# Optimization experiments

Measured on AMD Instinct MI355X. Metric: run time of the kernel, lower is better.

The kernel has to match this reference:

```python
import jax, jax.numpy as jnp
import numpy as np

B, N, C_X, D_MODEL, D_OUT, S = 32, 4096, 1, 64, 1, 2
D_IN = C_X + D_MODEL  # 65, channels entering graph_conv


def setup_inputs() -> dict:
    key = jax.random.key(0)
    ks = jax.random.split(key, 8)
    x = jax.random.normal(ks[0], (B, C_X, N), dtype=jnp.float32)
    h = jax.random.normal(ks[1], (B, D_MODEL, N), dtype=jnp.float32)
    # stacked support matrices (fwd/bwd normalized adjacency), used as a list of supports
    adj = jax.random.uniform(ks[2], (S, N, N), dtype=jnp.float32) / N
    # graph_conv.mlp : Conv2d(S*D_IN -> D_MODEL, 1x1)
    W_mlp = jax.random.normal(ks[3], (D_MODEL, S * D_IN), dtype=jnp.float32) / np.sqrt(S * D_IN)
    b_mlp = jnp.zeros((D_MODEL,), jnp.float32)
    # lin_out : Conv1d(2*D_MODEL -> D_MODEL, k=1)
    W_lin = jax.random.normal(ks[4], (D_MODEL, 2 * D_MODEL), dtype=jnp.float32) / np.sqrt(2 * D_MODEL)
    b_lin = jnp.zeros((D_MODEL,), jnp.float32)
    # read_out : Conv1d(2*D_MODEL -> D_OUT, k=1)
    W_read = jax.random.normal(ks[5], (D_OUT, 2 * D_MODEL), dtype=jnp.float32) / np.sqrt(2 * D_MODEL)
    b_read = jnp.zeros((D_OUT,), jnp.float32)
    prelu_a = jnp.array(0.25, jnp.float32)  # nn.PReLU() default: single shared slope
    return {"x": x, "h": h, "adj": adj, "W_mlp": W_mlp, "b_mlp": b_mlp,
            "W_lin": W_lin, "b_lin": b_lin, "W_read": W_read, "b_read": b_read,
            "prelu_a": prelu_a}


def conv1x1(W, b, x):
    # x: [B, C_in, N] -> [B, C_out, N]
    return jnp.einsum('oc,bcn->bon', W, x) + b[None, :, None]


def reference(x, h, adj, W_mlp, b_mlp, W_lin, b_lin, W_read, b_read, prelu_a):
    # x: [B, C_X, N], h: [B, D_MODEL, N], adj: [S, N, N]
    x_in = jnp.concatenate([x, h], axis=1)  # [B, D_IN, N]
    # SpatialConvOrderK (order=1, include_self=False):
    # out[b,c,w] per support s = sum_v x_in[b,c,v] * adj[s,w,v]
    hops = jnp.einsum('bcv,swv->bscw', x_in, adj)  # [B, S, D_IN, N]
    feats = hops.reshape(B, S * D_IN, N)           # channel-cat over supports
    out = conv1x1(W_mlp, b_mlp, feats)             # [B, D_MODEL, N]
    out = jnp.concatenate([out, h], axis=1)        # [B, 2*D_MODEL, N]
    out = conv1x1(W_lin, b_lin, out)               # [B, D_MODEL, N]
    out = jnp.where(out >= 0, out, prelu_a * out)  # PReLU
    out = jnp.concatenate([out, h], axis=1)        # [B, 2*D_MODEL, N]
    return (conv1x1(W_read, b_read, out), out)
```

## Files before the change

### kernel.cpp

```cpp
#include <hip/hip_runtime.h>
#include <cstdint>

#define N_NODES 4096
#define DM 64
#define K_DIM 8192
#define M_DIM 2048

typedef uint8_t u8;
using i32x8   = __attribute__((ext_vector_type(8))) int;
using floatx4 = __attribute__((ext_vector_type(4))) float;

#define GLOAD_LDS16(gp, lp)                                                     \
  __builtin_amdgcn_global_load_lds(                                             \
      reinterpret_cast<const __attribute__((address_space(1))) void*>(          \
          reinterpret_cast<uintptr_t>(gp)),                                     \
      reinterpret_cast<__attribute__((address_space(3))) void*>(                \
          (uint32_t)reinterpret_cast<uintptr_t>(lp)),                           \
      16, 0, 0)

__device__ inline int pk_fp8x4(float f0, float f1, float f2, float f3) {
  int r = __builtin_amdgcn_cvt_pk_fp8_f32(f0, f1, 0, false);
  r     = __builtin_amdgcn_cvt_pk_fp8_f32(f2, f3, r, true);
  return r;
}

__global__ __launch_bounds__(256) void k_prep(const float* __restrict__ adj,
                                              u8* __restrict__ BT8,
                                              const float* __restrict__ x,
                                              const float* __restrict__ h,
                                              const float* __restrict__ Wmlp,
                                              u8* __restrict__ A8) {
  __shared__ __align__(16) float Ws[DM * 68];
  uint32_t bi = blockIdx.x;
  if (bi >= 1024u) {
    const uint32_t lane = threadIdx.x & 63u;
    uint32_t gw = (bi - 1024u) * 4u + (threadIdx.x >> 6);
    for (uint32_t sc = gw; sc < 16384u; sc += 8192u) {
      const float4* src = reinterpret_cast<const float4*>(adj) + (size_t)sc * 512u + lane;
      float4 f[8];
#pragma unroll
      for (int q = 0; q < 8; ++q) f[q] = src[(size_t)q * 64];
      uint32_t row = sc >> 1;
      uint32_t s = row >> 12, w = row & 4095u;
      u8* dst = BT8 + (size_t)w * K_DIM + s * N_NODES + (sc & 1u) * 2048u + lane * 4u;
#pragma unroll
      for (int q = 0; q < 8; ++q) {
        int p = pk_fp8x4(f[q].x * 4096.f, f[q].y * 4096.f, f[q].z * 4096.f, f[q].w * 4096.f);
        *reinterpret_cast<int*>(dst + q * 256) = p;
      }
    }
    return;
  }
  uint32_t b2 = bi;
  uint32_t v0 = (b2 & 15u) * 256u;
  uint32_t s  = (b2 >> 4) & 1u;
  uint32_t b  = b2 >> 5;
  for (uint32_t t = threadIdx.x; t < DM * 68; t += 256) {
    uint32_t d = t / 68u, c = t % 68u;
    Ws[t] = (c < 65u) ? Wmlp[d * 130u + s * 65u + c] : 0.f;
  }
  __syncthreads();

  const uint32_t tv = threadIdx.x & 63u;
  const uint32_t td = threadIdx.x >> 6;
  const uint32_t v  = v0 + tv * 4u;

  float acc[16][4];
#pragma unroll
  for (int d = 0; d < 16; ++d)
#pragma unroll
    for (int k = 0; k < 4; ++k) acc[d][k] = 0.f;

  for (int c0 = 0; c0 < 64; c0 += 4) {
    float4 in4[4];
#pragma unroll
    for (int j = 0; j < 4; ++j) {
      int c = c0 + j;
      const float* src = (c == 0) ? (x + (size_t)b * N_NODES + v)
                                  : (h + ((size_t)b * DM + (c - 1)) * N_NODES + v);
      in4[j] = *reinterpret_cast<const float4*>(src);
    }
#pragma unroll
    for (int d = 0; d < 16; ++d) {
      const float4 w4 = *reinterpret_cast<const float4*>(&Ws[(td * 16 + d) * 68 + c0]);
      acc[d][0] += w4.x * in4[0].x + w4.y * in4[1].x + w4.z * in4[2].x + w4.w * in4[3].x;
      acc[d][1] += w4.x * in4[0].y + w4.y * in4[1].y + w4.z * in4[2].y + w4.w * in4[3].y;
      acc[d][2] += w4.x * in4[0].z + w4.y * in4[1].z + w4.z * in4[2].z + w4.w * in4[3].z;
      acc[d][3] += w4.x * in4[0].w + w4.y * in4[1].w + w4.z * in4[2].w + w4.w * in4[3].w;
    }
  }
  {
    float4 in4 = *reinterpret_cast<const float4*>(h + ((size_t)b * DM + 63) * N_NODES + v);
#pragma unroll
    for (int d = 0; d < 16; ++d) {
      float w = Ws[(td * 16 + d) * 68 + 64];
      acc[d][0] += w * in4.x; acc[d][1] += w * in4.y;
      acc[d][2] += w * in4.z; acc[d][3] += w * in4.w;
    }
  }
#pragma unroll
  for (int d = 0; d < 16; ++d) {
    int p = pk_fp8x4(acc[d][0], acc[d][1], acc[d][2], acc[d][3]);
    *reinterpret_cast<int*>(A8 + (size_t)(b * DM + td * 16 + d) * K_DIM + s * N_NODES + v) = p;
  }
}

__global__ void k_gemm(const u8* __restrict__ A, const u8* __restrict__ BT,
                       float* __restrict__ C) {
  __shared__ __align__(32) u8 As[4][128][32];
  __shared__ __align__(32) u8 Bs[4][128][32];
  const int tid  = threadIdx.x;
  const int lane = tid & 63;
  const int wave = tid >> 6;
  const int wr = wave >> 1, wc = wave & 1;
  const int m0 = blockIdx.y * 128, n0 = blockIdx.x * 128;
  const size_t kb = (size_t)blockIdx.z * 4096;

  const int srow = lane >> 1;
  const int shalf = (lane & 1) * 16;
  const u8* Ag = A  + (size_t)(m0 + wave * 32 + srow) * K_DIM + kb + shalf;
  const u8* Bg = BT + (size_t)(n0 + wave * 32 + srow) * K_DIM + kb + shalf;
  u8* AsB[4]; u8* BsB[4];
#pragma unroll
  for (int q = 0; q < 4; ++q) { AsB[q] = &As[q][wave * 32][0]; BsB[q] = &Bs[q][wave * 32][0]; }

  floatx4 acc[4][4];
#pragma unroll
  for (int i = 0; i < 4; ++i)
#pragma unroll
    for (int j = 0; j < 4; ++j) acc[i][j] = (floatx4){0.f, 0.f, 0.f, 0.f};

  const int fm = lane & 15;
  const int fq = lane >> 4;
  const int SC1 = 0x7F7F7F7F;

  for (int k0 = 0; k0 < 4096; k0 += 128) {
#pragma unroll
    for (int q = 0; q < 4; ++q) GLOAD_LDS16(Ag + k0 + q * 32, AsB[q]);
#pragma unroll
    for (int q = 0; q < 4; ++q) GLOAD_LDS16(Bg + k0 + q * 32, BsB[q]);
    __syncthreads();

    i32x8 af[4], bfr[4];
#pragma unroll
    for (int i = 0; i < 4; ++i)
      af[i] = *reinterpret_cast<const i32x8*>(&As[fq][wr * 64 + i * 16 + fm][0]);
#pragma unroll
    for (int j = 0; j < 4; ++j)
      bfr[j] = *reinterpret_cast<const i32x8*>(&Bs[fq][wc * 64 + j * 16 + fm][0]);
#pragma unroll
    for (int i = 0; i < 4; ++i)
#pragma unroll
      for (int j = 0; j < 4; ++j)
        acc[i][j] = __builtin_amdgcn_mfma_scale_f32_16x16x128_f8f6f4(
            af[i], bfr[j], acc[i][j], 0, 0, 0, SC1, 0, SC1);
    __syncthreads();
  }

  float* Cz = C + (size_t)blockIdx.z * M_DIM * N_NODES;
  const int cr = (lane >> 4) * 4;
  const int cc = lane & 15;
#pragma unroll
  for (int i = 0; i < 4; ++i)
#pragma unroll
    for (int j = 0; j < 4; ++j) {
      float* Cp = Cz + (size_t)(m0 + wr * 64 + i * 16 + cr) * N_NODES
                     + (n0 + wc * 64 + j * 16 + cc);
#pragma unroll
      for (int r = 0; r < 4; ++r) Cp[(size_t)r * N_NODES] = acc[i][j][r];
    }
}

__global__ __launch_bounds__(256) void k_epilogue(
    const float* __restrict__ C0, const float* __restrict__ C1,
    const float* __restrict__ h,
    const float* __restrict__ bmlp, const float* __restrict__ Wlin,
    const float* __restrict__ blin, const float* __restrict__ Wread,
    const float* __restrict__ bread, const float* __restrict__ pa,
    float* __restrict__ out0, float* __restrict__ out1) {
  __shared__ __align__(16) float sW[DM * 132];
  __shared__ float sbm[DM], sbl[DM], sWr[128];
  __shared__ float psum[3 * 256];
  for (uint32_t t = threadIdx.x; t < DM * 128; t += 256) {
    uint32_t d = t >> 7, c = t & 127u;
    sW[d * 132 + c] = Wlin[t];
  }
  if (threadIdx.x < DM) { sbm[threadIdx.x] = bmlp[threadIdx.x]; sbl[threadIdx.x] = blin[threadIdx.x]; }
  if (threadIdx.x < 128) sWr[threadIdx.x] = Wread[threadIdx.x];
  __syncthreads();

  uint32_t bi = blockIdx.x;
  uint32_t n0 = (bi & 15u) * 256u;
  uint32_t b  = bi >> 4;
  const uint32_t tv = threadIdx.x & 63u;
  const uint32_t td = threadIdx.x >> 6;
  const uint32_t n  = n0 + tv * 4u;
  const float KS = 1.0f / 4096.0f;

  float acc[16][4];
#pragma unroll
  for (int d = 0; d < 16; ++d) {
    float bl = sbl[td * 16 + d];
#pragma unroll
    for (int k = 0; k < 4; ++k) acc[d][k] = bl;
  }

  for (int c0 = 0; c0 < 64; c0 += 4) {
    float4 in4[4];
#pragma unroll
    for (int j = 0; j < 4; ++j) {
      size_t off = ((size_t)b * DM + (c0 + j)) * N_NODES + n;
      float4 v0 = *reinterpret_cast<const float4*>(C0 + off);
      float4 v1 = *reinterpret_cast<const float4*>(C1 + off);
      float bm = sbm[c0 + j];
      float4 v;
      v.x = (v0.x + v1.x) * KS + bm; v.y = (v0.y + v1.y) * KS + bm;
      v.z = (v0.z + v1.z) * KS + bm; v.w = (v0.w + v1.w) * KS + bm;
      in4[j] = v;
    }
#pragma unroll
    for (int d = 0; d < 16; ++d) {
      const float4 w4 = *reinterpret_cast<const float4*>(&sW[(td * 16 + d) * 132 + c0]);
      acc[d][0] += w4.x * in4[0].x + w4.y * in4[1].x + w4.z * in4[2].x + w4.w * in4[3].x;
      acc[d][1] += w4.x * in4[0].y + w4.y * in4[1].y + w4.z * in4[2].y + w4.w * in4[3].y;
      acc[d][2] += w4.x * in4[0].z + w4.y * in4[1].z + w4.z * in4[2].z + w4.w * in4[3].z;
      acc[d][3] += w4.x * in4[0].w + w4.y * in4[1].w + w4.z * in4[2].w + w4.w * in4[3].w;
    }
  }
  for (int c0 = 0; c0 < 64; c0 += 4) {
    float4 in4[4];
#pragma unroll
    for (int j = 0; j < 4; ++j)
      in4[j] = *reinterpret_cast<const float4*>(h + ((size_t)b * DM + (c0 + j)) * N_NODES + n);
#pragma unroll
    for (int d = 0; d < 16; ++d) {
      const float4 w4 = *reinterpret_cast<const float4*>(&sW[(td * 16 + d) * 132 + 64 + c0]);
      acc[d][0] += w4.x * in4[0].x + w4.y * in4[1].x + w4.z * in4[2].x + w4.w * in4[3].x;
      acc[d][1] += w4.x * in4[0].y + w4.y * in4[1].y + w4.z * in4[2].y + w4.w * in4[3].y;
      acc[d][2] += w4.x * in4[0].z + w4.y * in4[1].z + w4.z * in4[2].z + w4.w * in4[3].z;
      acc[d][3] += w4.x * in4[0].w + w4.y * in4[1].w + w4.z * in4[2].w + w4.w * in4[3].w;
    }
  }

  const float a = pa[0];
  float r[4] = {0.f, 0.f, 0.f, 0.f};
  float* o1b = out1 + (size_t)b * 128 * N_NODES + n;
#pragma unroll
  for (int d = 0; d < 16; ++d) {
    float4 o2;
    o2.x = acc[d][0] >= 0.f ? acc[d][0] : a * acc[d][0];
    o2.y = acc[d][1] >= 0.f ? acc[d][1] : a * acc[d][1];
    o2.z = acc[d][2] >= 0.f ? acc[d][2] : a * acc[d][2];
    o2.w = acc[d][3] >= 0.f ? acc[d][3] : a * acc[d][3];
    *reinterpret_cast<float4*>(o1b + (size_t)(td * 16 + d) * N_NODES) = o2;
    float wr = sWr[td * 16 + d];
    r[0] += wr * o2.x; r[1] += wr * o2.y; r[2] += wr * o2.z; r[3] += wr * o2.w;
  }
#pragma unroll
  for (int d = 0; d < 16; ++d) {
    float4 hv = *reinterpret_cast<const float4*>(h + ((size_t)b * DM + td * 16 + d) * N_NODES + n);
    *reinterpret_cast<float4*>(o1b + (size_t)(64 + td * 16 + d) * N_NODES) = hv;
    float wr = sWr[64 + td * 16 + d];
    r[0] += wr * hv.x; r[1] += wr * hv.y; r[2] += wr * hv.z; r[3] += wr * hv.w;
  }
  if (td > 0) {
#pragma unroll
    for (int k = 0; k < 4; ++k) psum[(td - 1) * 256 + tv * 4 + k] = r[k];
  }
  __syncthreads();
  if (td == 0) {
    float br = bread[0];
#pragma unroll
    for (int k = 0; k < 4; ++k)
      r[k] += br + psum[tv * 4 + k] + psum[256 + tv * 4 + k] + psum[512 + tv * 4 + k];
    float4 o0; o0.x = r[0]; o0.y = r[1]; o0.z = r[2]; o0.w = r[3];
    *reinterpret_cast<float4*>(out0 + (size_t)b * N_NODES + n) = o0;
  }
}

extern "C" void kernel_launch(void* const* d_in, const int* in_sizes, int n_in,
                              void* d_out, int out_size, void* d_ws, size_t ws_size,
                              hipStream_t stream) {
  const float* x     = (const float*)d_in[0];
  const float* h     = (const float*)d_in[1];
  const float* adj   = (const float*)d_in[2];
  const float* Wmlp  = (const float*)d_in[3];
  const float* bmlp  = (const float*)d_in[4];
  const float* Wlin  = (const float*)d_in[5];
  const float* blin  = (const float*)d_in[6];
  const float* Wread = (const float*)d_in[7];
  const float* bread = (const float*)d_in[8];
  const float* pa    = (const float*)d_in[9];

  char* ws = (char*)d_ws;
  u8*    Abuf  = (u8*)ws;
  u8*    BTbuf = (u8*)(ws + (16ull << 20));
  float* C0    = (float*)(ws + (48ull << 20));
  float* C1    = (float*)(ws + (80ull << 20));
  float* out0 = (float*)d_out;
  float* out1 = out0 + 131072;

  hipLaunchKernelGGL(k_prep,     dim3(3072),      dim3(256), 0, stream,
                     adj, BTbuf, x, h, Wmlp, Abuf);
  hipLaunchKernelGGL(k_gemm,     dim3(32, 16, 2), dim3(256), 0, stream, Abuf, BTbuf, C0);
  hipLaunchKernelGGL(k_epilogue, dim3(512),       dim3(256), 0, stream, C0, C1, h, bmlp,
                     Wlin, blin, Wread, bread, pa, out0, out1);
}
```

Baseline: 429.9 us.

## Fuse epilogue into fp8 GEMM and remove split-K intermediate buffers

Merges the per-node linear/PReLU/readout epilogue into the GEMM kernel, staging scaled GEMM outputs through reused LDS instead of writing two fp32 partial buffers to global memory. Split-K over two blocks is removed so each block covers the full K dimension, and block indices are swizzled. This cuts a large global write and read plus a kernel launch, at the cost of half as many GEMM blocks and a serialized epilogue per block.

New measurement: 441.2 us. 2.6% more time.

```diff
diff --git a/kernel.cpp b/kernel.cpp
--- a/kernel.cpp
+++ b/kernel.cpp
@@ -106,20 +106,41 @@
 }
 
 __global__ void k_gemm(const u8* __restrict__ A, const u8* __restrict__ BT,
-                       float* __restrict__ C) {
-  __shared__ __align__(32) u8 As[4][128][32];
-  __shared__ __align__(32) u8 Bs[4][128][32];
+                       const float* __restrict__ h,
+                       const float* __restrict__ bmlp, const float* __restrict__ Wlin,
+                       const float* __restrict__ blin, const float* __restrict__ Wread,
+                       const float* __restrict__ bread, const float* __restrict__ pa,
+                       float* __restrict__ out0, float* __restrict__ out1) {
+  __shared__ __align__(32) char smem[64 * 132 * 4];
+  __shared__ __align__(16) float sW[DM * 128];
+  __shared__ __align__(16) float sbm[DM], sbl[DM], sWr[128];
+  __shared__ __align__(16) float psum[8 * 128];
+
+  u8 (*As)[128][32] = reinterpret_cast<u8(*)[128][32]>(smem);
+  u8 (*Bs)[128][32] = reinterpret_cast<u8(*)[128][32]>(smem + 16384);
+  float (*gco)[132] = reinterpret_cast<float(*)[132]>(smem);
+
   const int tid  = threadIdx.x;
   const int lane = tid & 63;
   const int wave = tid >> 6;
   const int wr = wave >> 1, wc = wave & 1;
-  const int m0 = blockIdx.y * 128, n0 = blockIdx.x * 128;
-  const size_t kb = (size_t)blockIdx.z * 4096;
-
-  const int srow = lane >> 1;
+
+  uint32_t bi  = blockIdx.x;
+  uint32_t bi2 = (bi & 7u) * 64u + (bi >> 3);
+  const int xt = bi2 & 31, yt = bi2 >> 5;
+  const int m0 = yt * 128, n0 = xt * 128;
+  const int b0 = yt * 2;
+
+  for (int t = tid; t < DM * 128; t += 256) sW[t] = Wlin[t];
+  if (tid < DM)  { sbm[tid] = bmlp[tid]; sbl[tid] = blin[tid]; }
+  if (tid < 128) sWr[tid] = Wread[tid];
+  const float aP = pa[0];
+  const float br = bread[0];
+
+  const int srow  = lane >> 1;
   const int shalf = (lane & 1) * 16;
-  const u8* Ag = A  + (size_t)(m0 + wave * 32 + srow) * K_DIM + kb + shalf;
-  const u8* Bg = BT + (size_t)(n0 + wave * 32 + srow) * K_DIM + kb + shalf;
+  const u8* Ag = A  + (size_t)(m0 + wave * 32 + srow) * K_DIM + shalf;
+  const u8* Bg = BT + (size_t)(n0 + wave * 32 + srow) * K_DIM + shalf;
   u8* AsB[4]; u8* BsB[4];
 #pragma unroll
   for (int q = 0; q < 4; ++q) { AsB[q] = &As[q][wave * 32][0]; BsB[q] = &Bs[q][wave * 32][0]; }
@@ -134,7 +155,7 @@
   const int fq = lane >> 4;
   const int SC1 = 0x7F7F7F7F;
 
-  for (int k0 = 0; k0 < 4096; k0 += 128) {
+  for (int k0 = 0; k0 < 8192; k0 += 128) {
 #pragma unroll
     for (int q = 0; q < 4; ++q) GLOAD_LDS16(Ag + k0 + q * 32, AsB[q]);
 #pragma unroll
@@ -157,124 +178,112 @@
     __syncthreads();
   }
 
-  float* Cz = C + (size_t)blockIdx.z * M_DIM * N_NODES;
+  const float KS = 1.0f / 4096.0f;
   const int cr = (lane >> 4) * 4;
   const int cc = lane & 15;
-#pragma unroll
-  for (int i = 0; i < 4; ++i)
-#pragma unroll
-    for (int j = 0; j < 4; ++j) {
-      float* Cp = Cz + (size_t)(m0 + wr * 64 + i * 16 + cr) * N_NODES
-                     + (n0 + wc * 64 + j * 16 + cc);
-#pragma unroll
-      for (int r = 0; r < 4; ++r) Cp[(size_t)r * N_NODES] = acc[i][j][r];
-    }
-}
-
-__global__ __launch_bounds__(256) void k_epilogue(
-    const float* __restrict__ C0, const float* __restrict__ C1,
-    const float* __restrict__ h,
-    const float* __restrict__ bmlp, const float* __restrict__ Wlin,
-    const float* __restrict__ blin, const float* __restrict__ Wread,
-    const float* __restrict__ bread, const float* __restrict__ pa,
-    float* __restrict__ out0, float* __restrict__ out1) {
-  __shared__ __align__(16) float sW[DM * 132];
-  __shared__ float sbm[DM], sbl[DM], sWr[128];
-  __shared__ float psum[3 * 256];
-  for (uint32_t t = threadIdx.x; t < DM * 128; t += 256) {
-    uint32_t d = t >> 7, c = t & 127u;
-    sW[d * 132 + c] = Wlin[t];
-  }
-  if (threadIdx.x < DM) { sbm[threadIdx.x] = bmlp[threadIdx.x]; sbl[threadIdx.x] = blin[threadIdx.x]; }
-  if (threadIdx.x < 128) sWr[threadIdx.x] = Wread[threadIdx.x];
-  __syncthreads();
-
-  uint32_t bi = blockIdx.x;
-  uint32_t n0 = (bi & 15u) * 256u;
-  uint32_t b  = bi >> 4;
-  const uint32_t tv = threadIdx.x & 63u;
-  const uint32_t td = threadIdx.x >> 6;
-  const uint32_t n  = n0 + tv * 4u;
-  const float KS = 1.0f / 4096.0f;
-
-  float acc[16][4];
-#pragma unroll
-  for (int d = 0; d < 16; ++d) {
-    float bl = sbl[td * 16 + d];
-#pragma unroll
-    for (int k = 0; k < 4; ++k) acc[d][k] = bl;
-  }
-
-  for (int c0 = 0; c0 < 64; c0 += 4) {
-    float4 in4[4];
-#pragma unroll
-    for (int j = 0; j < 4; ++j) {
-      size_t off = ((size_t)b * DM + (c0 + j)) * N_NODES + n;
-      float4 v0 = *reinterpret_cast<const float4*>(C0 + off);
-      float4 v1 = *reinterpret_cast<const float4*>(C1 + off);
-      float bm = sbm[c0 + j];
-      float4 v;
-      v.x = (v0.x + v1.x) * KS + bm; v.y = (v0.y + v1.y) * KS + bm;
-      v.z = (v0.z + v1.z) * KS + bm; v.w = (v0.w + v1.w) * KS + bm;
-      in4[j] = v;
-    }
-#pragma unroll
-    for (int d = 0; d < 16; ++d) {
-      const float4 w4 = *reinterpret_cast<const float4*>(&sW[(td * 16 + d) * 132 + c0]);
-      acc[d][0] += w4.x * in4[0].x + w4.y * in4[1].x + w4.z * in4[2].x + w4.w * in4[3].x;
-      acc[d][1] += w4.x * in4[0].y + w4.y * in4[1].y + w4.z * in4[2].y + w4.w * in4[3].y;
-      acc[d][2] += w4.x * in4[0].z + w4.y * in4[1].z + w4.z * in4[2].z + w4.w * in4[3].z;
-      acc[d][3] += w4.x * in4[0].w + w4.y * in4[1].w + w4.z * in4[2].w + w4.w * in4[3].w;
-    }
-  }
-  for (int c0 = 0; c0 < 64; c0 += 4) {
-    float4 in4[4];
-#pragma unroll
-    for (int j = 0; j < 4; ++j)
-      in4[j] = *reinterpret_cast<const float4*>(h + ((size_t)b * DM + (c0 + j)) * N_NODES + n);
-#pragma unroll
-    for (int d = 0; d < 16; ++d) {
-      const float4 w4 = *reinterpret_cast<const float4*>(&sW[(td * 16 + d) * 132 + 64 + c0]);
-      acc[d][0] += w4.x * in4[0].x + w4.y * in4[1].x + w4.z * in4[2].x + w4.w * in4[3].x;
-      acc[d][1] += w4.x * in4[0].y + w4.y * in4[1].y + w4.z * in4[2].y + w4.w * in4[3].y;
-      acc[d][2] += w4.x * in4[0].z + w4.y * in4[1].z + w4.z * in4[2].z + w4.w * in4[3].z;
-      acc[d][3] += w4.x * in4[0].w + w4.y * in4[1].w + w4.z * in4[2].w + w4.w * in4[3].w;
-    }
-  }
-
-  const float a = pa[0];
-  float r[4] = {0.f, 0.f, 0.f, 0.f};
-  float* o1b = out1 + (size_t)b * 128 * N_NODES + n;
-#pragma unroll
-  for (int d = 0; d < 16; ++d) {
-    float4 o2;
-    o2.x = acc[d][0] >= 0.f ? acc[d][0] : a * acc[d][0];
-    o2.y = acc[d][1] >= 0.f ? acc[d][1] : a * acc[d][1];
-    o2.z = acc[d][2] >= 0.f ? acc[d][2] : a * acc[d][2];
-    o2.w = acc[d][3] >= 0.f ? acc[d][3] : a * acc[d][3];
-    *reinterpret_cast<float4*>(o1b + (size_t)(td * 16 + d) * N_NODES) = o2;
-    float wr = sWr[td * 16 + d];
-    r[0] += wr * o2.x; r[1] += wr * o2.y; r[2] += wr * o2.z; r[3] += wr * o2.w;
-  }
-#pragma unroll
-  for (int d = 0; d < 16; ++d) {
-    float4 hv = *reinterpret_cast<const float4*>(h + ((size_t)b * DM + td * 16 + d) * N_NODES + n);
-    *reinterpret_cast<float4*>(o1b + (size_t)(64 + td * 16 + d) * N_NODES) = hv;
-    float wr = sWr[64 + td * 16 + d];
-    r[0] += wr * hv.x; r[1] += wr * hv.y; r[2] += wr * hv.z; r[3] += wr * hv.w;
-  }
-  if (td > 0) {
-#pragma unroll
-    for (int k = 0; k < 4; ++k) psum[(td - 1) * 256 + tv * 4 + k] = r[k];
-  }
-  __syncthreads();
-  if (td == 0) {
-    float br = bread[0];
-#pragma unroll
-    for (int k = 0; k < 4; ++k)
-      r[k] += br + psum[tv * 4 + k] + psum[256 + tv * 4 + k] + psum[512 + tv * 4 + k];
-    float4 o0; o0.x = r[0]; o0.y = r[1]; o0.z = r[2]; o0.w = r[3];
-    *reinterpret_cast<float4*>(out0 + (size_t)b * N_NODES + n) = o0;
+  const int dsub = wave * 2 + (lane >> 5);
+  const int ncol = (lane & 31) * 4;
+
+  for (int p = 0; p < 2; ++p) {
+    if (wr == p) {
+#pragma unroll
+      for (int i = 0; i < 4; ++i)
+#pragma unroll
+        for (int j = 0; j < 4; ++j) {
+#pragma unroll
+          for (int r = 0; r < 4; ++r) {
+            int d = i * 16 + cr + r;
+            gco[d][wc * 64 + j * 16 + cc] = acc[i][j][r] * KS + sbm[d];
+          }
+        }
+    }
+    __syncthreads();
+
+    const int b = b0 + p;
+    float z[8][4];
+#pragma unroll
+    for (int dd = 0; dd < 8; ++dd) {
+      float bl = sbl[dsub * 8 + dd];
+#pragma unroll
+      for (int k = 0; k < 4; ++k) z[dd][k] = bl;
+    }
+
+    for (int k0 = 0; k0 < 64; k0 += 4) {
+      float4 g[4];
+#pragma unroll
+      for (int j = 0; j < 4; ++j)
+        g[j] = *reinterpret_cast<const float4*>(&gco[k0 + j][ncol]);
+#pragma unroll
+      for (int dd = 0; dd < 8; ++dd) {
+        const float4 w4 = *reinterpret_cast<const float4*>(&sW[(dsub * 8 + dd) * 128 + k0]);
+        z[dd][0] += w4.x * g[0].x + w4.y * g[1].x + w4.z * g[2].x + w4.w * g[3].x;
+        z[dd][1] += w4.x * g[0].y + w4.y * g[1].y + w4.z * g[2].y + w4.w * g[3].y;
+        z[dd][2] += w4.x * g[0].z + w4.y * g[1].z + w4.z * g[2].z + w4.w * g[3].z;
+        z[dd][3] += w4.x * g[0].w + w4.y * g[1].w + w4.z * g[2].w + w4.w * g[3].w;
+      }
+    }
+
+    const float* hb = h + (size_t)b * DM * N_NODES + n0 + ncol;
+    float* o1b = out1 + (size_t)b * 128 * N_NODES + n0 + ncol;
+    float hs[4] = {0.f, 0.f, 0.f, 0.f};
+    for (int k0 = 0; k0 < 64; k0 += 4) {
+      float4 hv[4];
+#pragma unroll
+      for (int j = 0; j < 4; ++j)
+        hv[j] = *reinterpret_cast<const float4*>(hb + (size_t)(k0 + j) * N_NODES);
+#pragma unroll
+      for (int dd = 0; dd < 8; ++dd) {
+        const float4 w4 = *reinterpret_cast<const float4*>(&sW[(dsub * 8 + dd) * 128 + 64 + k0]);
+        z[dd][0] += w4.x * hv[0].x + w4.y * hv[1].x + w4.z * hv[2].x + w4.w * hv[3].x;
+        z[dd][1] += w4.x * hv[0].y + w4.y * hv[1].y + w4.z * hv[2].y + w4.w * hv[3].y;
+        z[dd][2] += w4.x * hv[0].z + w4.y * hv[1].z + w4.z * hv[2].z + w4.w * hv[3].z;
+        z[dd][3] += w4.x * hv[0].w + w4.y * hv[1].w + w4.z * hv[2].w + w4.w * hv[3].w;
+      }
+      if (dsub == 0) {
+#pragma unroll
+        for (int j = 0; j < 4; ++j) {
+          *reinterpret_cast<float4*>(o1b + (size_t)(64 + k0 + j) * N_NODES) = hv[j];
+          float w = sWr[64 + k0 + j];
+          hs[0] += w * hv[j].x; hs[1] += w * hv[j].y;
+          hs[2] += w * hv[j].z; hs[3] += w * hv[j].w;
+        }
+      }
+    }
+
+    float rp[4] = {0.f, 0.f, 0.f, 0.f};
+#pragma unroll
+    for (int dd = 0; dd < 8; ++dd) {
+      int dp = dsub * 8 + dd;
+      float4 o2;
+      o2.x = z[dd][0] >= 0.f ? z[dd][0] : aP * z[dd][0];
+      o2.y = z[dd][1] >= 0.f ? z[dd][1] : aP * z[dd][1];
+      o2.z = z[dd][2] >= 0.f ? z[dd][2] : aP * z[dd][2];
+      o2.w = z[dd][3] >= 0.f ? z[dd][3] : aP * z[dd][3];
+      *reinterpret_cast<float4*>(o1b + (size_t)dp * N_NODES) = o2;
+      float w = sWr[dp];
+      rp[0] += w * o2.x; rp[1] += w * o2.y; rp[2] += w * o2.z; rp[3] += w * o2.w;
+    }
+    if (dsub == 0) {
+      rp[0] += hs[0]; rp[1] += hs[1]; rp[2] += hs[2]; rp[3] += hs[3];
+    }
+    {
+      float4 rv; rv.x = rp[0]; rv.y = rp[1]; rv.z = rp[2]; rv.w = rp[3];
+      *reinterpret_cast<float4*>(&psum[dsub * 128 + ncol]) = rv;
+    }
+    __syncthreads();
+    if (wave == 0 && lane < 32) {
+      float s0[4];
+#pragma unroll
+      for (int k = 0; k < 4; ++k) {
+        float s = br;
+#pragma unroll
+        for (int ds = 0; ds < 8; ++ds) s += psum[ds * 128 + ncol + k];
+        s0[k] = s;
+      }
+      float4 ov; ov.x = s0[0]; ov.y = s0[1]; ov.z = s0[2]; ov.w = s0[3];
+      *reinterpret_cast<float4*>(out0 + (size_t)b * N_NODES + n0 + ncol) = ov;
+    }
+    __syncthreads();
   }
 }
 
@@ -295,14 +304,11 @@
   char* ws = (char*)d_ws;
   u8*    Abuf  = (u8*)ws;
   u8*    BTbuf = (u8*)(ws + (16ull << 20));
-  float* C0    = (float*)(ws + (48ull << 20));
-  float* C1    = (float*)(ws + (80ull << 20));
   float* out0 = (float*)d_out;
   float* out1 = out0 + 131072;
 
-  hipLaunchKernelGGL(k_prep,     dim3(3072),      dim3(256), 0, stream,
+  hipLaunchKernelGGL(k_prep, dim3(3072), dim3(256), 0, stream,
                      adj, BTbuf, x, h, Wmlp, Abuf);
-  hipLaunchKernelGGL(k_gemm,     dim3(32, 16, 2), dim3(256), 0, stream, Abuf, BTbuf, C0);
-  hipLaunchKernelGGL(k_epilogue, dim3(512),       dim3(256), 0, stream, C0, C1, h, bmlp,
-                     Wlin, blin, Wread, bread, pa, out0, out1);
+  hipLaunchKernelGGL(k_gemm, dim3(512),  dim3(256), 0, stream,
+                     Abuf, BTbuf, h, bmlp, Wlin, blin, Wread, bread, pa, out0, out1);
 }
```
